# Kernel tuning notes

Measured on AMD Instinct MI355X. Metric: run time of the kernel, lower is better.

The kernel has to match this reference:

```python
import jax, jax.numpy as jnp
import numpy as np
import math

B, S, D, H = 8, 1024, 1024, 16
HD = D // H  # head_features = 64
SCALE = math.sqrt(HD)


def setup_inputs() -> dict:
    key = jax.random.key(0)
    k0, k1, k2, k3, k4 = jax.random.split(key, 5)
    x = jax.random.normal(k0, (B, S, D), dtype=jnp.float32)
    attn_mask = (jax.random.uniform(k1, (B, S, S)) < 0.9).astype(jnp.float32)
    w_scale = 1.0 / math.sqrt(D)  # keep unsafe exp in finite range
    Wq = jax.random.normal(k2, (D, D), dtype=jnp.float32) * w_scale
    Wk = jax.random.normal(k3, (D, D), dtype=jnp.float32) * w_scale
    Wv = jax.random.normal(k4, (D, D), dtype=jnp.float32) * w_scale
    return {"x": x, "attn_mask": attn_mask, "Wq": Wq, "Wk": Wk, "Wv": Wv}


def reference(x, attn_mask, Wq, Wk, Wv):
    b, s, _ = x.shape

    def split_heads(t):  # [b,s,D] -> [b,H,s,HD]
        return t.reshape(b, s, H, HD).transpose(0, 2, 1, 3)

    q = split_heads(x @ Wq)
    k = split_heads(x @ Wk)
    v = split_heads(x @ Wv)

    # unsafe softmax: exp without max subtraction, multiplicative mask, +1e-8 denom
    scores = jnp.einsum('bhsd,bhtd->bhst', q, k) / SCALE
    e = jnp.exp(scores) * attn_mask[:, None, :, :]
    w = e / (e.sum(axis=3, keepdims=True) + 1e-8)

    ctx = jnp.einsum('bhst,bhtd->bhsd', w, v)  # [b,H,s,HD]
    return ctx.transpose(0, 2, 1, 3).reshape(b, s, D)
```

## Files before the change

kernel.cpp:

```cpp
#include <hip/hip_runtime.h>

#define KDIM 1024

typedef _Float16 half8 __attribute__((ext_vector_type(8)));
typedef _Float16 half4 __attribute__((ext_vector_type(4)));
typedef float f32x4 __attribute__((ext_vector_type(4)));

#if defined(__has_builtin)
#if __has_builtin(__builtin_amdgcn_global_load_lds)
#define HAVE_GLDS 1
#endif
#endif

__device__ __forceinline__ void stage16(const _Float16* g, _Float16* wave_base, int lane) {
#ifdef HAVE_GLDS
  __builtin_amdgcn_global_load_lds(
      (const __attribute__((address_space(1))) void*)g,
      (__attribute__((address_space(3))) void*)wave_base, 16, 0, 0);
#else
  *(half8*)(wave_base + lane * 8) = *(const half8*)g;
#endif
}

__global__ void cast_x_kernel(const float* __restrict__ x, _Float16* __restrict__ xb) {
  size_t i = ((size_t)blockIdx.x * 256 + threadIdx.x) * 4;
  float4 v = *(const float4*)(x + i);
  half4 h = { (_Float16)v.x, (_Float16)v.y, (_Float16)v.z, (_Float16)v.w };
  *(half4*)(xb + i) = h;
}

__global__ void wtrans_kernel(const float* __restrict__ Wq, const float* __restrict__ Wk,
                              const float* __restrict__ Wv, _Float16* __restrict__ Wqkvt) {
  int z = blockIdx.z;
  const float* src = z == 0 ? Wq : (z == 1 ? Wk : Wv);
  _Float16* dst = Wqkvt + (size_t)z * KDIM * KDIM;
  float sc = (z == 0) ? 0.125f : 1.0f;
  __shared__ _Float16 tile[32][33];
  int tx = threadIdx.x & 31, ty = threadIdx.x >> 5;
  int c0 = blockIdx.x * 32, r0 = blockIdx.y * 32;
#pragma unroll
  for (int i = 0; i < 4; i++) {
    int r = r0 + ty + i * 8;
    tile[tx][ty + i * 8] = (_Float16)(src[(size_t)r * KDIM + c0 + tx] * sc);
  }
  __syncthreads();
#pragma unroll
  for (int i = 0; i < 4; i++) {
    int n = c0 + ty + i * 8;
    dst[(size_t)n * KDIM + r0 + tx] = tile[ty + i * 8][tx];
  }
}

__global__ void maskbits_kernel(const float* __restrict__ m, unsigned long long* __restrict__ bits) {
  size_t i = (size_t)blockIdx.x * 256 + threadIdx.x;
  unsigned long long b = __ballot(m[i] != 0.0f);
  if ((threadIdx.x & 63) == 0) bits[i >> 6] = b;
}

__global__ __launch_bounds__(256, 2)
void gemm_kernel(const _Float16* __restrict__ A, const _Float16* __restrict__ Bt,
                 _Float16* __restrict__ Qt, _Float16* __restrict__ Kh,
                 _Float16* __restrict__ Vth) {
  __shared__ _Float16 As[128 * 32];
  __shared__ _Float16 Bs[128 * 32];
  int tid = threadIdx.x;
  int lane = tid & 63, w4 = tid >> 6;
  int la = lane & 15, qd = lane >> 4;
  int wm = w4 & 1, wn = w4 >> 1;
  int m0 = blockIdx.y * 128, n0 = blockIdx.x * 128;
  int r = tid >> 2, c = (tid & 3) * 8;
  const _Float16* Ag = A + (size_t)(m0 + r) * KDIM + c;
  const _Float16* Bg = Bt + (size_t)(n0 + r) * KDIM + c;
  _Float16* a0 = As + w4 * 512;
  _Float16* b0 = Bs + w4 * 512;
  f32x4 acc[4][4] = {};
  for (int kt = 0; kt < KDIM; kt += 32) {
    stage16(Ag + kt, a0, lane);
    stage16(Ag + (size_t)64 * KDIM + kt, a0 + 2048, lane);
    stage16(Bg + kt, b0, lane);
    stage16(Bg + (size_t)64 * KDIM + kt, b0 + 2048, lane);
    __syncthreads();
    half8 af[4], bf[4];
#pragma unroll
    for (int mi = 0; mi < 4; mi++)
      af[mi] = *(const half8*)(As + (wm * 64 + mi * 16 + la) * 32 + qd * 8);
#pragma unroll
    for (int ni = 0; ni < 4; ni++)
      bf[ni] = *(const half8*)(Bs + (wn * 64 + ni * 16 + la) * 32 + qd * 8);
#pragma unroll
    for (int mi = 0; mi < 4; mi++)
#pragma unroll
      for (int ni = 0; ni < 4; ni++)
        acc[mi][ni] = __builtin_amdgcn_mfma_f32_16x16x32_f16(af[mi], bf[ni], acc[mi][ni], 0, 0, 0);
    __syncthreads();
  }
  int which = n0 >> 10;
  int hh = ((n0 + wn * 64) >> 6) & 15;
  int mbase = m0 + wm * 64;
  int b = mbase >> 10, s0 = mbase & 1023;
  if (which == 1) {
#pragma unroll
    for (int mi = 0; mi < 4; mi++)
#pragma unroll
      for (int ni = 0; ni < 4; ni++) {
        f32x4 v = acc[mi][ni];
        int s = s0 + mi * 16 + qd * 4;
        int d = ni * 16 + la;
#pragma unroll
        for (int rg = 0; rg < 4; rg++)
          Kh[(((size_t)(b * 16 + hh)) * 1024 + s + rg) * 64 + d] = (_Float16)v[rg];
      }
  } else {
    _Float16* dst = (which == 0) ? Qt : Vth;
    _Float16* ep = (w4 < 2) ? (As + w4 * 2048) : (Bs + (w4 - 2) * 2048);
    _Float16* base = dst + ((size_t)(b * 16 + hh)) * 64 * 1024;
    int rr = lane >> 2, c4 = lane & 3;
#pragma unroll
    for (int ni = 0; ni < 4; ni++) {
#pragma unroll
      for (int mi = 0; mi < 4; mi++) {
        f32x4 v = acc[mi][ni];
        half4 hv = { (_Float16)v[0], (_Float16)v[1], (_Float16)v[2], (_Float16)v[3] };
        *(half4*)(ep + la * 72 + mi * 16 + qd * 4) = hv;
      }
      half8 o0 = *(const half8*)(ep + rr * 72 + c4 * 16);
      half8 o1 = *(const half8*)(ep + rr * 72 + c4 * 16 + 8);
      _Float16* gp = base + (size_t)(ni * 16 + rr) * 1024 + s0 + c4 * 16;
      *(half8*)gp = o0;
      *(half8*)(gp + 8) = o1;
    }
  }
}

__global__ __launch_bounds__(256, 4)
void attn_kernel(const _Float16* __restrict__ Qt, const _Float16* __restrict__ K,
                 const _Float16* __restrict__ Vt, const unsigned long long* __restrict__ mbits,
                 float* __restrict__ out) {
  __shared__ _Float16 Ks[2 * 64 * 32];
  __shared__ _Float16 Vs[2 * 64 * 40];
  int tid = threadIdx.x;
  int lane = tid & 63, w4 = tid >> 6;
  int la = lane & 15, qd = lane >> 4;
  int linear = blockIdx.x;
  int xlo = linear & 7;
  int tmp = linear >> 3;
  int qt = tmp & 15;
  int hb = (tmp >> 4) * 8 + xlo;
  int h = hb & 15, b = hb >> 4;
  const _Float16* Qp = Qt + ((size_t)(b * 16 + h)) * 64 * 1024;
  const _Float16* Kp = K + ((size_t)(b * 16 + h)) * 1024 * 64;
  const _Float16* Vp = Vt + ((size_t)(b * 16 + h)) * 64 * 1024;
  int q0w = qt * 64 + w4 * 16;
  half8 qf[2];
#pragma unroll
  for (int ks = 0; ks < 2; ks++)
#pragma unroll
    for (int j = 0; j < 8; j++)
      qf[ks][j] = Qp[(size_t)(ks * 32 + qd * 8 + j) * 1024 + q0w + la];
  unsigned long long mq[4];
  {
    const ulonglong2* mp =
        (const ulonglong2*)(mbits + ((size_t)b * 1024 + q0w + la) * 16 + qd * 4);
    ulonglong2 m01 = mp[0];
    ulonglong2 m23 = mp[1];
    mq[0] = m01.x; mq[1] = m01.y; mq[2] = m23.x; mq[3] = m23.y;
  }
  f32x4 acco[4] = {};
  float rs = 0.0f;
  int r = tid >> 2, c = (tid & 3) * 8;
  _Float16* kbase = Ks + w4 * 512;
  for (int tt = 0; tt < 16; tt++) {
    half8 v0 = *(const half8*)(Vp + (size_t)r * 1024 + tt * 64 + c);
    half8 v1 = *(const half8*)(Vp + (size_t)r * 1024 + tt * 64 + 32 + c);
    stage16(Kp + (size_t)(tt * 64 + r) * 64 + c, kbase, lane);
    stage16(Kp + (size_t)(tt * 64 + r) * 64 + 32 + c, kbase + 2048, lane);
    *(half8*)(Vs + r * 40 + c) = v0;
    *(half8*)(Vs + 2560 + r * 40 + c) = v1;
    __syncthreads();
    f32x4 accs[4] = {};
#pragma unroll
    for (int tsub = 0; tsub < 4; tsub++)
#pragma unroll
      for (int ks = 0; ks < 2; ks++) {
        half8 kf = *(const half8*)(Ks + ks * 2048 + (tsub * 16 + la) * 32 + qd * 8);
        accs[tsub] = __builtin_amdgcn_mfma_f32_16x16x32_f16(kf, qf[ks], accs[tsub], 0, 0, 0);
      }
    unsigned long long mw = __shfl(mq[tt & 3], ((tt >> 2) << 4) + la);
#pragma unroll
    for (int tsub = 0; tsub < 4; tsub++) {
      half4 pf;
#pragma unroll
      for (int rg = 0; rg < 4; rg++) {
        float e = ((mw >> (tsub * 16 + qd * 4 + rg)) & 1ull) ? __expf(accs[tsub][rg]) : 0.0f;
        rs += e;
        pf[rg] = (_Float16)e;
      }
#pragma unroll
      for (int nsub = 0; nsub < 4; nsub++) {
        half4 vf = *(const half4*)(Vs + (tsub >> 1) * 2560 + (nsub * 16 + la) * 40 +
                                   (tsub & 1) * 16 + qd * 4);
        acco[nsub] = __builtin_amdgcn_mfma_f32_16x16x16f16(pf, vf, acco[nsub], 0, 0, 0);
      }
    }
    __syncthreads();
  }
  rs += __shfl_xor(rs, 16);
  rs += __shfl_xor(rs, 32);
  float inv_q = 1.0f / (rs + 1e-8f);
  float* op = out + (size_t)b * 1024 * 1024 + (size_t)h * 64;
#pragma unroll
  for (int rg = 0; rg < 4; rg++) {
    float inv = __shfl(inv_q, qd * 4 + rg);
    int s = q0w + qd * 4 + rg;
#pragma unroll
    for (int nsub = 0; nsub < 4; nsub++)
      op[(size_t)s * 1024 + nsub * 16 + la] = acco[nsub][rg] * inv;
  }
}

extern "C" void kernel_launch(void* const* d_in, const int* in_sizes, int n_in,
                              void* d_out, int out_size, void* d_ws, size_t ws_size,
                              hipStream_t stream) {
  (void)in_sizes; (void)n_in; (void)out_size; (void)ws_size;
  const float* x = (const float*)d_in[0];
  const float* am = (const float*)d_in[1];
  const float* Wq = (const float*)d_in[2];
  const float* Wk = (const float*)d_in[3];
  const float* Wv = (const float*)d_in[4];
  float* out = (float*)d_out;

  char* p = (char*)d_ws;
  _Float16* xb = (_Float16*)p;    p += (size_t)8192 * 1024 * 2;
  _Float16* Wqkvt = (_Float16*)p; p += (size_t)3 * 1024 * 1024 * 2;
  _Float16* Qt = (_Float16*)p;    p += (size_t)8192 * 1024 * 2;
  _Float16* Kh = (_Float16*)p;    p += (size_t)8192 * 1024 * 2;
  _Float16* Vth = (_Float16*)p;   p += (size_t)8192 * 1024 * 2;
  unsigned long long* mb = (unsigned long long*)p;

  cast_x_kernel<<<8192, 256, 0, stream>>>(x, xb);
  wtrans_kernel<<<dim3(32, 32, 3), 256, 0, stream>>>(Wq, Wk, Wv, Wqkvt);
  maskbits_kernel<<<32768, 256, 0, stream>>>(am, mb);
  gemm_kernel<<<dim3(24, 64), 256, 0, stream>>>(xb, Wqkvt, Qt, Kh, Vth);
  attn_kernel<<<2048, 256, 0, stream>>>(Qt, Kh, Vth, mb, out);
}
```

Baseline: 260.8 us.

## Share K/V tiles across 8 waves and fold log2e into Q for exp2

The attention kernel now launches 512-thread blocks, with 8 waves covering 128 queries and sharing one staged 64-key K/V tile. Each thread issues a single K and a single V load per step, which halves global and LDS staging traffic per query. The log2(e) factor is folded into the Wq scaling so the softmax can use the hardware exp2. Probabilities are packed with cvt_pkrtz and the row sum is taken with fdot2 on the packed fp16 values. In exchange, occupancy is reduced to 2 blocks of 512 threads, and the row sums now use round-toward-zero fp16 values, which slightly changes precision.

New measurement: 266.2 us. 2.1% more time.

```diff
diff --git a/kernel.cpp b/kernel.cpp
--- a/kernel.cpp
+++ b/kernel.cpp
@@ -4,12 +4,26 @@
 
 typedef _Float16 half8 __attribute__((ext_vector_type(8)));
 typedef _Float16 half4 __attribute__((ext_vector_type(4)));
+typedef __fp16 fp16x2 __attribute__((ext_vector_type(2)));
+typedef __fp16 fp16x4 __attribute__((ext_vector_type(4)));
 typedef float f32x4 __attribute__((ext_vector_type(4)));
 
 #if defined(__has_builtin)
 #if __has_builtin(__builtin_amdgcn_global_load_lds)
 #define HAVE_GLDS 1
 #endif
+#if __has_builtin(__builtin_amdgcn_exp2f)
+#define EXP2(x) __builtin_amdgcn_exp2f(x)
+#endif
+#if __has_builtin(__builtin_amdgcn_cvt_pkrtz)
+#define HAVE_PKRTZ 1
+#endif
+#if __has_builtin(__builtin_amdgcn_fdot2)
+#define HAVE_FDOT2 1
+#endif
+#endif
+#ifndef EXP2
+#define EXP2(x) exp2f(x)
 #endif
 
 __device__ __forceinline__ void stage16(const _Float16* g, _Float16* wave_base, int lane) {
@@ -34,7 +48,7 @@
   int z = blockIdx.z;
   const float* src = z == 0 ? Wq : (z == 1 ? Wk : Wv);
   _Float16* dst = Wqkvt + (size_t)z * KDIM * KDIM;
-  float sc = (z == 0) ? 0.125f : 1.0f;
+  float sc = (z == 0) ? 0.18033688011112042f : 1.0f;
   __shared__ _Float16 tile[32][33];
   int tx = threadIdx.x & 31, ty = threadIdx.x >> 5;
   int c0 = blockIdx.x * 32, r0 = blockIdx.y * 32;
@@ -132,7 +146,7 @@
   }
 }
 
-__global__ __launch_bounds__(256, 4)
+__global__ __launch_bounds__(512, 2)
 void attn_kernel(const _Float16* __restrict__ Qt, const _Float16* __restrict__ K,
                  const _Float16* __restrict__ Vt, const unsigned long long* __restrict__ mbits,
                  float* __restrict__ out) {
@@ -144,13 +158,13 @@
   int linear = blockIdx.x;
   int xlo = linear & 7;
   int tmp = linear >> 3;
-  int qt = tmp & 15;
-  int hb = (tmp >> 4) * 8 + xlo;
+  int qt = tmp & 7;
+  int hb = (tmp >> 3) * 8 + xlo;
   int h = hb & 15, b = hb >> 4;
   const _Float16* Qp = Qt + ((size_t)(b * 16 + h)) * 64 * 1024;
   const _Float16* Kp = K + ((size_t)(b * 16 + h)) * 1024 * 64;
   const _Float16* Vp = Vt + ((size_t)(b * 16 + h)) * 64 * 1024;
-  int q0w = qt * 64 + w4 * 16;
+  int q0w = qt * 128 + w4 * 16;
   half8 qf[2];
 #pragma unroll
   for (int ks = 0; ks < 2; ks++)
@@ -167,15 +181,19 @@
   }
   f32x4 acco[4] = {};
   float rs = 0.0f;
-  int r = tid >> 2, c = (tid & 3) * 8;
+  int kt_t = (tid & 255) >> 2;
+  int kt_d = (tid >> 8) * 32 + (tid & 3) * 8;
   _Float16* kbase = Ks + w4 * 512;
+  int vd = tid >> 3;
+  int vt = (tid & 7) * 8;
+  _Float16* vdst = Vs + (vt >= 32 ? 2560 : 0) + vd * 40 + (vt & 31);
+#ifdef HAVE_FDOT2
+  fp16x2 one2 = { (__fp16)1.0f, (__fp16)1.0f };
+#endif
   for (int tt = 0; tt < 16; tt++) {
-    half8 v0 = *(const half8*)(Vp + (size_t)r * 1024 + tt * 64 + c);
-    half8 v1 = *(const half8*)(Vp + (size_t)r * 1024 + tt * 64 + 32 + c);
-    stage16(Kp + (size_t)(tt * 64 + r) * 64 + c, kbase, lane);
-    stage16(Kp + (size_t)(tt * 64 + r) * 64 + 32 + c, kbase + 2048, lane);
-    *(half8*)(Vs + r * 40 + c) = v0;
-    *(half8*)(Vs + 2560 + r * 40 + c) = v1;
+    half8 vv = *(const half8*)(Vp + (size_t)vd * 1024 + tt * 64 + vt);
+    stage16(Kp + (size_t)(tt * 64 + kt_t) * 64 + kt_d, kbase, lane);
+    *(half8*)vdst = vv;
     __syncthreads();
     f32x4 accs[4] = {};
 #pragma unroll
@@ -188,13 +206,25 @@
     unsigned long long mw = __shfl(mq[tt & 3], ((tt >> 2) << 4) + la);
 #pragma unroll
     for (int tsub = 0; tsub < 4; tsub++) {
+      float e0 = ((mw >> (tsub * 16 + qd * 4 + 0)) & 1ull) ? EXP2(accs[tsub][0]) : 0.0f;
+      float e1 = ((mw >> (tsub * 16 + qd * 4 + 1)) & 1ull) ? EXP2(accs[tsub][1]) : 0.0f;
+      float e2 = ((mw >> (tsub * 16 + qd * 4 + 2)) & 1ull) ? EXP2(accs[tsub][2]) : 0.0f;
+      float e3 = ((mw >> (tsub * 16 + qd * 4 + 3)) & 1ull) ? EXP2(accs[tsub][3]) : 0.0f;
       half4 pf;
-#pragma unroll
-      for (int rg = 0; rg < 4; rg++) {
-        float e = ((mw >> (tsub * 16 + qd * 4 + rg)) & 1ull) ? __expf(accs[tsub][rg]) : 0.0f;
-        rs += e;
-        pf[rg] = (_Float16)e;
-      }
+#ifdef HAVE_PKRTZ
+      fp16x2 p01 = __builtin_amdgcn_cvt_pkrtz(e0, e1);
+      fp16x2 p23 = __builtin_amdgcn_cvt_pkrtz(e2, e3);
+      fp16x4 pfv = __builtin_shufflevector(p01, p23, 0, 1, 2, 3);
+      pf = __builtin_bit_cast(half4, pfv);
+#else
+      pf[0] = (_Float16)e0; pf[1] = (_Float16)e1; pf[2] = (_Float16)e2; pf[3] = (_Float16)e3;
+#endif
+#if defined(HAVE_FDOT2) && defined(HAVE_PKRTZ)
+      rs = __builtin_amdgcn_fdot2(p01, one2, rs, false);
+      rs = __builtin_amdgcn_fdot2(p23, one2, rs, false);
+#else
+      rs += e0 + e1 + e2 + e3;
+#endif
 #pragma unroll
       for (int nsub = 0; nsub < 4; nsub++) {
         half4 vf = *(const half4*)(Vs + (tsub >> 1) * 2560 + (nsub * 16 + la) * 40 +
@@ -241,5 +271,5 @@
   wtrans_kernel<<<dim3(32, 32, 3), 256, 0, stream>>>(Wq, Wk, Wv, Wqkvt);
   maskbits_kernel<<<32768, 256, 0, stream>>>(am, mb);
   gemm_kernel<<<dim3(24, 64), 256, 0, stream>>>(xb, Wqkvt, Qt, Kh, Vth);
-  attn_kernel<<<2048, 256, 0, stream>>>(Qt, Kh, Vth, mb, out);
-}
+  attn_kernel<<<1024, 512, 0, stream>>>(Qt, Kh, Vth, mb, out);
+}
```
